# Optimization experiments

Measured on AMD Instinct MI355X. Metric: run time of the kernel, lower is better.

The kernel has to match this reference:

```python
import jax, jax.numpy as jnp
import numpy as np


def setup_inputs() -> dict:
    key = jax.random.key(0)
    ks = jax.random.split(key, 10)
    B, S, H = 8192, 8, 256
    SD, PD, AD = 9, 2, 7

    def lin(k, fan_in, shape):
        bound = 1.0 / np.sqrt(fan_in)
        return jax.random.uniform(k, shape, jnp.float32, -bound, bound)

    return {
        "state": jax.random.normal(ks[0], (B, SD), jnp.float32),
        "proprio": jax.random.normal(ks[1], (B, PD), jnp.float32),
        "target_pos": jax.random.normal(ks[2], (B, 3), jnp.float32),
        "noise": jax.random.normal(ks[3], (S, B, AD), jnp.float32),
        # action_proposal: Linear(11,H) -> ReLU -> Linear(H,7) -> Tanh
        "pw1": lin(ks[4], SD + PD, (SD + PD, H)),
        "pb1": jnp.zeros((H,), jnp.float32),
        "pw2": lin(ks[5], H, (H, AD)),
        "pb2": jnp.zeros((AD,), jnp.float32),
        # forward_model: Linear(16,H) -> ReLU -> Linear(H,H) -> ReLU -> Linear(H,9)
        "w1": lin(ks[6], SD + AD, (SD + AD, H)),
        "b1": jnp.zeros((H,), jnp.float32),
        "w2": lin(ks[7], H, (H, H)),
        "b2": jnp.zeros((H,), jnp.float32),
        "w3": lin(ks[8], H, (H, SD)),
        "b3": jnp.zeros((SD,), jnp.float32),
        "horizon": 4,
    }


def reference(state, proprio, target_pos, noise, pw1, pb1, pw2, pb2,
              w1, b1, w2, b2, w3, b3, horizon):
    # action proposal
    x = jnp.concatenate([state, proprio], axis=-1)          # (B, 11)
    base_action = jnp.tanh(jax.nn.relu(x @ pw1 + pb1) @ pw2 + pb2)  # (B, 7)

    # candidates for all samples at once (vectorizes the num_samples loop)
    cand = jnp.clip(base_action[None] + 0.2 * noise, -1.0, 1.0)      # (S, B, 7)

    S = cand.shape[0]
    sim0 = jnp.broadcast_to(state[None], (S,) + state.shape)         # (S, B, 9)

    def step(carry, _):
        sim, total = carry
        inp = jnp.concatenate([sim, cand], axis=-1)                  # (S, B, 16)
        h = jax.nn.relu(inp @ w1 + b1)
        h = jax.nn.relu(h @ w2 + b2)
        sim = h @ w3 + b3                                            # (S, B, 9)
        cost = jnp.sum((sim[..., :3] - target_pos[None]) ** 2, axis=-1)  # (S, B)
        return (sim, total + cost), None

    total0 = jnp.zeros(cand.shape[:2], jnp.float32)
    (_, total_cost), _ = jax.lax.scan(step, (sim0, total0), None, length=horizon)

    # masked best-cost update with strict '<' against +inf == first-argmin over samples
    best = jnp.argmin(total_cost, axis=0)                            # (B,)
    best_actions = jnp.take_along_axis(cand, best[None, :, None], axis=0)[0]  # (B, 7)
    return best_actions
```

## Files before the change

### kernel.cpp

```cpp
#include <hip/hip_runtime.h>
#include <math.h>

#define NSD 9
#define NPD 2
#define NAD 7
#define NH  256
#define NIN 16
#define LOSCALE 2048.0f
#define LOINV   (1.0f / 2048.0f)

typedef _Float16 half8 __attribute__((ext_vector_type(8)));
typedef float    floatx4 __attribute__((ext_vector_type(4)));


__device__ __forceinline__ void stage16(const _Float16* g, _Float16* l)
{
    __builtin_amdgcn_global_load_lds(
        (const __attribute__((address_space(1))) void*)g,
        (__attribute__((address_space(3))) void*)l, 16, 0, 0);
}

__global__ __launch_bounds__(64) void k_packW(
    const float* __restrict__ w1, const float* __restrict__ b1,
    const float* __restrict__ w2, const float* __restrict__ w3,
    _Float16* __restrict__ pc, _Float16* __restrict__ p3)
{
    const int bid  = blockIdx.x;
    const int lane = threadIdx.x;
    const int q = lane >> 4, ln = lane & 15;
    half8 hv, lv;
    _Float16* dst;
    if (bid < 16) {
        const int t = bid;
        const int c = 32*(t>>1) + 8*(ln>>2) + 4*(t&1) + (ln&3);
#pragma unroll
        for (int j = 0; j < 8; ++j) {
            const int k = 8*q + j;
            const float x = (k < NIN) ? w1[k*NH + c]
                                      : (k == NIN ? b1[c] : 0.0f);
            const _Float16 h = (_Float16)x;
            hv[j] = h; lv[j] = (_Float16)((x - (float)h) * LOSCALE);
        }
        dst = pc + (size_t)(t >> 1) * 18432 + 16384 + (size_t)(t & 1) * 1024;
    } else if (bid < 144) {
        const int idx = bid - 16, t = idx >> 3, kc = idx & 7;
        const int c = 32*(t>>1) + 8*(ln>>2) + 4*(t&1) + (ln&3);
#pragma unroll
        for (int j = 0; j < 8; ++j) {
            const int k = kc*32 + 8*q + j;
            const float x = w2[k*NH + c];
            const _Float16 h = (_Float16)x;
            hv[j] = h; lv[j] = (_Float16)((x - (float)h) * LOSCALE);
        }
        dst = pc + (size_t)kc * 18432 + (size_t)t * 1024;
    } else {
        const int kc = bid - 144;
#pragma unroll
        for (int j = 0; j < 8; ++j) {
            const int k = kc*32 + 8*q + j;
            const float x = (ln < NSD) ? w3[k*NSD + ln] : 0.0f;
            const _Float16 h = (_Float16)x;
            hv[j] = h; lv[j] = (_Float16)((x - (float)h) * LOSCALE);
        }
        dst = p3 + (size_t)kc * 1024;
    }
    *(half8*)&dst[lane*8]       = hv;
    *(half8*)&dst[512 + lane*8] = lv;
}

__global__ __launch_bounds__(256) void k_proposal(
    const float* __restrict__ state, const float* __restrict__ proprio,
    const float* __restrict__ noise, const float* __restrict__ pw1,
    const float* __restrict__ pb1, const float* __restrict__ pw2,
    const float* __restrict__ pb2, float* __restrict__ cand, int B)
{
    const int wave = threadIdx.x >> 6;
    const int lane = threadIdx.x & 63;
    const int b = blockIdx.x * 4 + wave;
    if (b >= B) return;

    float x[11];
#pragma unroll
    for (int k = 0; k < 9; ++k) x[k] = state[b * NSD + k];
    x[9]  = proprio[b * NPD + 0];
    x[10] = proprio[b * NPD + 1];

    float hc[4];
#pragma unroll
    for (int i = 0; i < 4; ++i) {
        const int c = lane + 64 * i;
        float acc = pb1[c];
#pragma unroll
        for (int k = 0; k < 11; ++k) acc = fmaf(x[k], pw1[k * NH + c], acc);
        hc[i] = fmaxf(acc, 0.0f);
    }

    float base[7];
#pragma unroll
    for (int j = 0; j < 7; ++j) {
        float p = 0.0f;
#pragma unroll
        for (int i = 0; i < 4; ++i)
            p = fmaf(hc[i], pw2[(lane + 64 * i) * NAD + j], p);
#pragma unroll
        for (int off = 32; off >= 1; off >>= 1) p += __shfl_xor(p, off, 64);
        base[j] = tanhf(p + pb2[j]);
    }

    if (lane < 8 * NAD) {
        const int s = lane / NAD, j = lane % NAD;
        float bj = base[0];
#pragma unroll
        for (int jj = 1; jj < 7; ++jj) if (j == jj) bj = base[jj];
        float v = bj + 0.2f * noise[((size_t)s * B + b) * NAD + j];
        v = fminf(fmaxf(v, -1.0f), 1.0f);
        cand[((size_t)s * B + b) * NAD + j] = v;
    }
}

__global__ __launch_bounds__(256, 2) void k_rollout(
    const float* __restrict__ state, const float* __restrict__ target,
    const float* __restrict__ cand,
    const _Float16* __restrict__ pc, const _Float16* __restrict__ p3,
    const float* __restrict__ b2, const float* __restrict__ b3,
    const int* __restrict__ hor_ptr, float* __restrict__ cost, int B)
{
    __shared__ _Float16 sb[2][18432];
    __shared__ float inpL[4][16][20];
    __shared__ float b2L[NH];

    const int tid  = threadIdx.x;
    const int wv   = tid >> 6;
    const int lane = tid & 63;
    const int q = lane >> 4, ln = lane & 15;
    const int chunk = blockIdx.x * 4 + wv;
    const int p0 = chunk * 16;
    const int s  = p0 / B;
    const int b0 = p0 % B;
    const int horizon = *hor_ptr;

    auto STAGE = [&](int buf, int kc) {
        const _Float16* gbase = pc + (size_t)kc * 18432 + tid * 8;
        _Float16* lbase = &sb[buf][wv * 512];
#pragma unroll
        for (int i = 0; i < 9; ++i)
            stage16(gbase + i * 2048, lbase + i * 2048);
    };

    b2L[tid] = b2[tid];
    if (q == 0) {
        float* row = &inpL[wv][ln][0];
        const int b = b0 + ln;
#pragma unroll
        for (int k = 0; k < NSD; ++k) row[k] = state[b * NSD + k];
#pragma unroll
        for (int j = 0; j < NAD; ++j)
            row[NSD + j] = cand[((size_t)s * B + b) * NAD + j];
        row[16] = 1.0f; row[17] = 0.0f; row[18] = 0.0f; row[19] = 0.0f;
    }
    float tg[3] = {0.0f, 0.0f, 0.0f};
    if (q == 0) {
#pragma unroll
        for (int r = 0; r < 3; ++r) tg[r] = target[(b0 + ln) * 3 + r];
    }
    float b3v[4];
#pragma unroll
    for (int r = 0; r < 4; ++r) {
        const int f = q * 4 + r;
        b3v[r] = (f < NSD) ? b3[f] : 0.0f;
    }
    float costAcc = 0.0f;

    STAGE(0, 0);
    asm volatile("s_waitcnt vmcnt(0)" ::: "memory");
    __syncthreads();
    int cur = 0;

    const floatx4 z4 = {0.0f, 0.0f, 0.0f, 0.0f};

    for (int h = 0; h < horizon; ++h) {
        const float* row = &inpL[wv][ln][0];
        float4 fa = {0, 0, 0, 0}, fb = {0, 0, 0, 0};
        if (q < 3) fa = *(const float4*)&row[8 * q];
        if (q < 2) fb = *(const float4*)&row[8 * q + 4];
        half8 bh, bl;
        {
            const float vv[8] = {fa.x, fa.y, fa.z, fa.w, fb.x, fb.y, fb.z, fb.w};
#pragma unroll
            for (int j = 0; j < 8; ++j) {
                const _Float16 hh = (_Float16)vv[j];
                bh[j] = hh;
                bl[j] = (_Float16)((vv[j] - (float)hh) * LOSCALE);
            }
        }

        floatx4 C1[16], C2[16];
#pragma unroll
        for (int t = 0; t < 16; ++t) { C1[t] = z4; C2[t] = z4; }

        for (int kc = 0; kc < 8; ++kc) {
            const int nkc = (kc < 7) ? kc + 1 : 0;
            STAGE(cur ^ 1, nkc);

            half8 h1h, h1l;
            {
                const half8 a1h0 = *(const half8*)&sb[cur][16384 + lane*8];
                const half8 a1l0 = *(const half8*)&sb[cur][16384 + 512 + lane*8];
                const half8 a1h1 = *(const half8*)&sb[cur][16384 + 1024 + lane*8];
                const half8 a1l1 = *(const half8*)&sb[cur][16384 + 1536 + lane*8];
                floatx4 c1t = __builtin_amdgcn_mfma_f32_16x16x32_f16(a1h0, bh, z4, 0, 0, 0);
                floatx4 c2t = __builtin_amdgcn_mfma_f32_16x16x32_f16(a1h0, bl, z4, 0, 0, 0);
                c2t = __builtin_amdgcn_mfma_f32_16x16x32_f16(a1l0, bh, c2t, 0, 0, 0);
#pragma unroll
                for (int r = 0; r < 4; ++r) {
                    const float v = fmaxf(fmaf(c2t[r], LOINV, c1t[r]), 0.0f);
                    const _Float16 hh = (_Float16)v;
                    h1h[r] = hh;
                    h1l[r] = (_Float16)((v - (float)hh) * LOSCALE);
                }
                c1t = __builtin_amdgcn_mfma_f32_16x16x32_f16(a1h1, bh, z4, 0, 0, 0);
                c2t = __builtin_amdgcn_mfma_f32_16x16x32_f16(a1h1, bl, z4, 0, 0, 0);
                c2t = __builtin_amdgcn_mfma_f32_16x16x32_f16(a1l1, bh, c2t, 0, 0, 0);
#pragma unroll
                for (int r = 0; r < 4; ++r) {
                    const float v = fmaxf(fmaf(c2t[r], LOINV, c1t[r]), 0.0f);
                    const _Float16 hh = (_Float16)v;
                    h1h[4 + r] = hh;
                    h1l[4 + r] = (_Float16)((v - (float)hh) * LOSCALE);
                }
            }

#pragma unroll
            for (int t = 0; t < 16; ++t) {
                const half8 a2h = *(const half8*)&sb[cur][t * 1024 + lane * 8];
                const half8 a2l = *(const half8*)&sb[cur][t * 1024 + 512 + lane * 8];
                C1[t] = __builtin_amdgcn_mfma_f32_16x16x32_f16(a2h, h1h, C1[t], 0, 0, 0);
                C2[t] = __builtin_amdgcn_mfma_f32_16x16x32_f16(a2h, h1l, C2[t], 0, 0, 0);
                C2[t] = __builtin_amdgcn_mfma_f32_16x16x32_f16(a2l, h1h, C2[t], 0, 0, 0);
            }

            __syncthreads();
            cur ^= 1;
        }

        floatx4 D1 = z4, D2 = z4;
        half8 h2h, h2l;
#pragma unroll
        for (int t = 0; t < 16; ++t) {
            const float4 bb = *(const float4*)&b2L[32*(t>>1) + 8*q + 4*(t&1)];
            const float bbv[4] = {bb.x, bb.y, bb.z, bb.w};
#pragma unroll
            for (int r = 0; r < 4; ++r) {
                const float v = fmaxf(C1[t][r] + LOINV * C2[t][r] + bbv[r], 0.0f);
                const _Float16 hh = (_Float16)v;
                h2h[(t & 1) * 4 + r] = hh;
                h2l[(t & 1) * 4 + r] = (_Float16)((v - (float)hh) * LOSCALE);
            }
            if (t & 1) {
                const int kc2 = t >> 1;
                const half8 a3h = *(const half8*)&p3[(size_t)kc2 * 1024 + lane*8];
                const half8 a3l = *(const half8*)&p3[(size_t)kc2 * 1024 + 512 + lane*8];
                D1 = __builtin_amdgcn_mfma_f32_16x16x32_f16(a3h, h2h, D1, 0, 0, 0);
                D2 = __builtin_amdgcn_mfma_f32_16x16x32_f16(a3h, h2l, D2, 0, 0, 0);
                D2 = __builtin_amdgcn_mfma_f32_16x16x32_f16(a3l, h2h, D2, 0, 0, 0);
            }
        }
        float v[4];
#pragma unroll
        for (int r = 0; r < 4; ++r)
            v[r] = D1[r] + LOINV * D2[r] + b3v[r];

        if (q == 0) {
            const float d0 = v[0] - tg[0], d1 = v[1] - tg[1], d2 = v[2] - tg[2];
            costAcc += d0 * d0 + d1 * d1 + d2 * d2;
        }
        if (q < 2) {
            const float4 w4 = {v[0], v[1], v[2], v[3]};
            *(float4*)&inpL[wv][ln][4 * q] = w4;
        } else if (q == 2) {
            inpL[wv][ln][8] = v[0];
        }
        asm volatile("s_waitcnt lgkmcnt(0)" ::: "memory");
    }

    if (q == 0) cost[(size_t)s * B + b0 + ln] = costAcc;
}

__global__ __launch_bounds__(256) void k_select(
    const float* __restrict__ cost, const float* __restrict__ cand,
    float* __restrict__ out, int B, int S)
{
    const int b = blockIdx.x * 256 + threadIdx.x;
    if (b >= B) return;
    float best = cost[b];
    int bs = 0;
    for (int s = 1; s < S; ++s) {
        const float c = cost[(size_t)s * B + b];
        if (c < best) { best = c; bs = s; }
    }
#pragma unroll
    for (int j = 0; j < NAD; ++j)
        out[b * NAD + j] = cand[((size_t)bs * B + b) * NAD + j];
}

extern "C" void kernel_launch(void* const* d_in, const int* in_sizes, int n_in,
                              void* d_out, int out_size, void* d_ws, size_t ws_size,
                              hipStream_t stream)
{
    const float* state   = (const float*)d_in[0];
    const float* proprio = (const float*)d_in[1];
    const float* target  = (const float*)d_in[2];
    const float* noise   = (const float*)d_in[3];
    const float* pw1     = (const float*)d_in[4];
    const float* pb1     = (const float*)d_in[5];
    const float* pw2     = (const float*)d_in[6];
    const float* pb2     = (const float*)d_in[7];
    const float* w1      = (const float*)d_in[8];
    const float* b1      = (const float*)d_in[9];
    const float* w2      = (const float*)d_in[10];
    const float* b2      = (const float*)d_in[11];
    const float* w3      = (const float*)d_in[12];
    const float* b3      = (const float*)d_in[13];
    const int*   horizon = (const int*)d_in[14];

    const int B = in_sizes[0] / NSD;
    const int S = in_sizes[3] / (B * NAD);

    float* cand = (float*)d_ws;
    float* cost = cand + (size_t)S * B * NAD;
    _Float16* pc = (_Float16*)(cost + (size_t)S * B);
    _Float16* p3 = pc + 8 * 18432;
    float* out  = (float*)d_out;

    k_packW<<<dim3(152), dim3(64), 0, stream>>>(w1, b1, w2, w3, pc, p3);
    k_proposal<<<dim3((B + 3) / 4), dim3(256), 0, stream>>>(
        state, proprio, noise, pw1, pb1, pw2, pb2, cand, B);
    k_rollout<<<dim3((S * B) / 64), dim3(256), 0, stream>>>(
        state, target, cand, pc, p3, b2, b3, horizon, cost, B);
    k_select<<<dim3((B + 255) / 256), dim3(256), 0, stream>>>(
        cost, cand, out, B, S);
}
```

Measured before the change: 221.7 us.

## Split layer-2 columns across wave pairs and merge weight-pack with proposal kernel

Each pair of waves now works on both waves' 16-sample chunks but only half of the 16 output tiles of the 256x256 layer. Each A-fragment loaded from LDS is therefore reused for two B operands, which halves LDS weight reads per MFMA. The partial layer-3 outputs are exchanged through shared memory with extra barriers each horizon step. Separately, the weight-packing and action-proposal kernels are fused into one launch to save a kernel launch.

```diff
diff --git a/kernel.cpp b/kernel.cpp
--- a/kernel.cpp
+++ b/kernel.cpp
@@ -8,6 +8,7 @@
 #define NIN 16
 #define LOSCALE 2048.0f
 #define LOINV   (1.0f / 2048.0f)
+#define NPACKB 152
 
 typedef _Float16 half8 __attribute__((ext_vector_type(8)));
 typedef float    floatx4 __attribute__((ext_vector_type(4)));
@@ -20,63 +21,65 @@
         (__attribute__((address_space(3))) void*)l, 16, 0, 0);
 }
 
-__global__ __launch_bounds__(64) void k_packW(
+__global__ __launch_bounds__(256) void k_prep(
     const float* __restrict__ w1, const float* __restrict__ b1,
     const float* __restrict__ w2, const float* __restrict__ w3,
-    _Float16* __restrict__ pc, _Float16* __restrict__ p3)
-{
-    const int bid  = blockIdx.x;
-    const int lane = threadIdx.x;
-    const int q = lane >> 4, ln = lane & 15;
-    half8 hv, lv;
-    _Float16* dst;
-    if (bid < 16) {
-        const int t = bid;
-        const int c = 32*(t>>1) + 8*(ln>>2) + 4*(t&1) + (ln&3);
-#pragma unroll
-        for (int j = 0; j < 8; ++j) {
-            const int k = 8*q + j;
-            const float x = (k < NIN) ? w1[k*NH + c]
-                                      : (k == NIN ? b1[c] : 0.0f);
-            const _Float16 h = (_Float16)x;
-            hv[j] = h; lv[j] = (_Float16)((x - (float)h) * LOSCALE);
-        }
-        dst = pc + (size_t)(t >> 1) * 18432 + 16384 + (size_t)(t & 1) * 1024;
-    } else if (bid < 144) {
-        const int idx = bid - 16, t = idx >> 3, kc = idx & 7;
-        const int c = 32*(t>>1) + 8*(ln>>2) + 4*(t&1) + (ln&3);
-#pragma unroll
-        for (int j = 0; j < 8; ++j) {
-            const int k = kc*32 + 8*q + j;
-            const float x = w2[k*NH + c];
-            const _Float16 h = (_Float16)x;
-            hv[j] = h; lv[j] = (_Float16)((x - (float)h) * LOSCALE);
-        }
-        dst = pc + (size_t)kc * 18432 + (size_t)t * 1024;
-    } else {
-        const int kc = bid - 144;
-#pragma unroll
-        for (int j = 0; j < 8; ++j) {
-            const int k = kc*32 + 8*q + j;
-            const float x = (ln < NSD) ? w3[k*NSD + ln] : 0.0f;
-            const _Float16 h = (_Float16)x;
-            hv[j] = h; lv[j] = (_Float16)((x - (float)h) * LOSCALE);
-        }
-        dst = p3 + (size_t)kc * 1024;
-    }
-    *(half8*)&dst[lane*8]       = hv;
-    *(half8*)&dst[512 + lane*8] = lv;
-}
-
-__global__ __launch_bounds__(256) void k_proposal(
+    _Float16* __restrict__ pc, _Float16* __restrict__ p3,
     const float* __restrict__ state, const float* __restrict__ proprio,
     const float* __restrict__ noise, const float* __restrict__ pw1,
     const float* __restrict__ pb1, const float* __restrict__ pw2,
     const float* __restrict__ pb2, float* __restrict__ cand, int B)
 {
+    const int bid = blockIdx.x;
+    if (bid < NPACKB) {
+        if (threadIdx.x >= 64) return;
+        const int lane = threadIdx.x;
+        const int q = lane >> 4, ln = lane & 15;
+        half8 hv, lv;
+        _Float16* dst;
+        if (bid < 16) {
+            const int t = bid;
+            const int c = 32*(t>>1) + 8*(ln>>2) + 4*(t&1) + (ln&3);
+#pragma unroll
+            for (int j = 0; j < 8; ++j) {
+                const int k = 8*q + j;
+                const float x = (k < NIN) ? w1[k*NH + c]
+                                          : (k == NIN ? b1[c] : 0.0f);
+                const _Float16 h = (_Float16)x;
+                hv[j] = h; lv[j] = (_Float16)((x - (float)h) * LOSCALE);
+            }
+            dst = pc + (size_t)(t >> 1) * 18432 + 16384 + (size_t)(t & 1) * 1024;
+        } else if (bid < 144) {
+            const int idx = bid - 16, t = idx >> 3, kc = idx & 7;
+            const int c = 32*(t>>1) + 8*(ln>>2) + 4*(t&1) + (ln&3);
+#pragma unroll
+            for (int j = 0; j < 8; ++j) {
+                const int k = kc*32 + 8*q + j;
+                const float x = w2[k*NH + c];
+                const _Float16 h = (_Float16)x;
+                hv[j] = h; lv[j] = (_Float16)((x - (float)h) * LOSCALE);
+            }
+            dst = pc + (size_t)kc * 18432 + (size_t)t * 1024;
+        } else {
+            const int kc = bid - 144;
+#pragma unroll
+            for (int j = 0; j < 8; ++j) {
+                const int k = kc*32 + 8*q + j;
+                const float x = (ln < NSD) ? w3[k*NSD + ln] : 0.0f;
+                const _Float16 h = (_Float16)x;
+                hv[j] = h; lv[j] = (_Float16)((x - (float)h) * LOSCALE);
+            }
+            dst = p3 + (size_t)kc * 1024;
+        }
+        *(half8*)&dst[lane*8]       = hv;
+        *(half8*)&dst[512 + lane*8] = lv;
+        return;
+    }
+
+    const int pbid = bid - NPACKB;
     const int wave = threadIdx.x >> 6;
     const int lane = threadIdx.x & 63;
-    const int b = blockIdx.x * 4 + wave;
+    const int b = pbid * 4 + wave;
     if (b >= B) return;
 
     float x[11];
@@ -133,6 +136,9 @@
     const int wv   = tid >> 6;
     const int lane = tid & 63;
     const int q = lane >> 4, ln = lane & 15;
+    const int wpair = wv & 2;
+    const int gown  = wv & 1;
+    const int tbase = gown * 8;
     const int chunk = blockIdx.x * 4 + wv;
     const int p0 = chunk * 16;
     const int s  = p0 / B;
@@ -179,96 +185,132 @@
     const floatx4 z4 = {0.0f, 0.0f, 0.0f, 0.0f};
 
     for (int h = 0; h < horizon; ++h) {
-        const float* row = &inpL[wv][ln][0];
-        float4 fa = {0, 0, 0, 0}, fb = {0, 0, 0, 0};
-        if (q < 3) fa = *(const float4*)&row[8 * q];
-        if (q < 2) fb = *(const float4*)&row[8 * q + 4];
-        half8 bh, bl;
-        {
+        half8 bh[2], bl[2];
+#pragma unroll
+        for (int g = 0; g < 2; ++g) {
+            const float* row = &inpL[wpair + g][ln][0];
+            float4 fa = {0, 0, 0, 0}, fb = {0, 0, 0, 0};
+            if (q < 3) fa = *(const float4*)&row[8 * q];
+            if (q < 2) fb = *(const float4*)&row[8 * q + 4];
             const float vv[8] = {fa.x, fa.y, fa.z, fa.w, fb.x, fb.y, fb.z, fb.w};
 #pragma unroll
             for (int j = 0; j < 8; ++j) {
                 const _Float16 hh = (_Float16)vv[j];
-                bh[j] = hh;
-                bl[j] = (_Float16)((vv[j] - (float)hh) * LOSCALE);
-            }
-        }
-
-        floatx4 C1[16], C2[16];
-#pragma unroll
-        for (int t = 0; t < 16; ++t) { C1[t] = z4; C2[t] = z4; }
+                bh[g][j] = hh;
+                bl[g][j] = (_Float16)((vv[j] - (float)hh) * LOSCALE);
+            }
+        }
+
+        floatx4 C1[8][2], C2[8][2];
+#pragma unroll
+        for (int tt = 0; tt < 8; ++tt)
+#pragma unroll
+            for (int g = 0; g < 2; ++g) { C1[tt][g] = z4; C2[tt][g] = z4; }
 
         for (int kc = 0; kc < 8; ++kc) {
             const int nkc = (kc < 7) ? kc + 1 : 0;
             STAGE(cur ^ 1, nkc);
 
-            half8 h1h, h1l;
-            {
-                const half8 a1h0 = *(const half8*)&sb[cur][16384 + lane*8];
-                const half8 a1l0 = *(const half8*)&sb[cur][16384 + 512 + lane*8];
-                const half8 a1h1 = *(const half8*)&sb[cur][16384 + 1024 + lane*8];
-                const half8 a1l1 = *(const half8*)&sb[cur][16384 + 1536 + lane*8];
-                floatx4 c1t = __builtin_amdgcn_mfma_f32_16x16x32_f16(a1h0, bh, z4, 0, 0, 0);
-                floatx4 c2t = __builtin_amdgcn_mfma_f32_16x16x32_f16(a1h0, bl, z4, 0, 0, 0);
-                c2t = __builtin_amdgcn_mfma_f32_16x16x32_f16(a1l0, bh, c2t, 0, 0, 0);
+            const half8 a1h0 = *(const half8*)&sb[cur][16384 + lane*8];
+            const half8 a1l0 = *(const half8*)&sb[cur][16384 + 512 + lane*8];
+            const half8 a1h1 = *(const half8*)&sb[cur][16384 + 1024 + lane*8];
+            const half8 a1l1 = *(const half8*)&sb[cur][16384 + 1536 + lane*8];
+            half8 h1h[2], h1l[2];
+#pragma unroll
+            for (int g = 0; g < 2; ++g) {
+                floatx4 c1t = __builtin_amdgcn_mfma_f32_16x16x32_f16(a1h0, bh[g], z4, 0, 0, 0);
+                floatx4 c2t = __builtin_amdgcn_mfma_f32_16x16x32_f16(a1h0, bl[g], z4, 0, 0, 0);
+                c2t = __builtin_amdgcn_mfma_f32_16x16x32_f16(a1l0, bh[g], c2t, 0, 0, 0);
 #pragma unroll
                 for (int r = 0; r < 4; ++r) {
                     const float v = fmaxf(fmaf(c2t[r], LOINV, c1t[r]), 0.0f);
                     const _Float16 hh = (_Float16)v;
-                    h1h[r] = hh;
-                    h1l[r] = (_Float16)((v - (float)hh) * LOSCALE);
-                }
-                c1t = __builtin_amdgcn_mfma_f32_16x16x32_f16(a1h1, bh, z4, 0, 0, 0);
-                c2t = __builtin_amdgcn_mfma_f32_16x16x32_f16(a1h1, bl, z4, 0, 0, 0);
-                c2t = __builtin_amdgcn_mfma_f32_16x16x32_f16(a1l1, bh, c2t, 0, 0, 0);
+                    h1h[g][r] = hh;
+                    h1l[g][r] = (_Float16)((v - (float)hh) * LOSCALE);
+                }
+                c1t = __builtin_amdgcn_mfma_f32_16x16x32_f16(a1h1, bh[g], z4, 0, 0, 0);
+                c2t = __builtin_amdgcn_mfma_f32_16x16x32_f16(a1h1, bl[g], z4, 0, 0, 0);
+                c2t = __builtin_amdgcn_mfma_f32_16x16x32_f16(a1l1, bh[g], c2t, 0, 0, 0);
 #pragma unroll
                 for (int r = 0; r < 4; ++r) {
                     const float v = fmaxf(fmaf(c2t[r], LOINV, c1t[r]), 0.0f);
                     const _Float16 hh = (_Float16)v;
-                    h1h[4 + r] = hh;
-                    h1l[4 + r] = (_Float16)((v - (float)hh) * LOSCALE);
-                }
-            }
-
-#pragma unroll
-            for (int t = 0; t < 16; ++t) {
+                    h1h[g][4 + r] = hh;
+                    h1l[g][4 + r] = (_Float16)((v - (float)hh) * LOSCALE);
+                }
+            }
+
+#pragma unroll
+            for (int tt = 0; tt < 8; ++tt) {
+                const int t = tbase + tt;
                 const half8 a2h = *(const half8*)&sb[cur][t * 1024 + lane * 8];
                 const half8 a2l = *(const half8*)&sb[cur][t * 1024 + 512 + lane * 8];
-                C1[t] = __builtin_amdgcn_mfma_f32_16x16x32_f16(a2h, h1h, C1[t], 0, 0, 0);
-                C2[t] = __builtin_amdgcn_mfma_f32_16x16x32_f16(a2h, h1l, C2[t], 0, 0, 0);
-                C2[t] = __builtin_amdgcn_mfma_f32_16x16x32_f16(a2l, h1h, C2[t], 0, 0, 0);
+#pragma unroll
+                for (int g = 0; g < 2; ++g) {
+                    C1[tt][g] = __builtin_amdgcn_mfma_f32_16x16x32_f16(a2h, h1h[g], C1[tt][g], 0, 0, 0);
+                    C2[tt][g] = __builtin_amdgcn_mfma_f32_16x16x32_f16(a2h, h1l[g], C2[tt][g], 0, 0, 0);
+                    C2[tt][g] = __builtin_amdgcn_mfma_f32_16x16x32_f16(a2l, h1h[g], C2[tt][g], 0, 0, 0);
+                }
             }
 
             __syncthreads();
             cur ^= 1;
         }
 
-        floatx4 D1 = z4, D2 = z4;
-        half8 h2h, h2l;
-#pragma unroll
-        for (int t = 0; t < 16; ++t) {
+        floatx4 D1[2] = {z4, z4}, D2[2] = {z4, z4};
+        half8 h2h[2], h2l[2];
+#pragma unroll
+        for (int tt = 0; tt < 8; ++tt) {
+            const int t = tbase + tt;
             const float4 bb = *(const float4*)&b2L[32*(t>>1) + 8*q + 4*(t&1)];
             const float bbv[4] = {bb.x, bb.y, bb.z, bb.w};
 #pragma unroll
-            for (int r = 0; r < 4; ++r) {
-                const float v = fmaxf(C1[t][r] + LOINV * C2[t][r] + bbv[r], 0.0f);
-                const _Float16 hh = (_Float16)v;
-                h2h[(t & 1) * 4 + r] = hh;
-                h2l[(t & 1) * 4 + r] = (_Float16)((v - (float)hh) * LOSCALE);
-            }
-            if (t & 1) {
+            for (int g = 0; g < 2; ++g)
+#pragma unroll
+                for (int r = 0; r < 4; ++r) {
+                    const float v = fmaxf(C1[tt][g][r] + LOINV * C2[tt][g][r] + bbv[r], 0.0f);
+                    const _Float16 hh = (_Float16)v;
+                    h2h[g][(tt & 1) * 4 + r] = hh;
+                    h2l[g][(tt & 1) * 4 + r] = (_Float16)((v - (float)hh) * LOSCALE);
+                }
+            if (tt & 1) {
                 const int kc2 = t >> 1;
                 const half8 a3h = *(const half8*)&p3[(size_t)kc2 * 1024 + lane*8];
                 const half8 a3l = *(const half8*)&p3[(size_t)kc2 * 1024 + 512 + lane*8];
-                D1 = __builtin_amdgcn_mfma_f32_16x16x32_f16(a3h, h2h, D1, 0, 0, 0);
-                D2 = __builtin_amdgcn_mfma_f32_16x16x32_f16(a3h, h2l, D2, 0, 0, 0);
-                D2 = __builtin_amdgcn_mfma_f32_16x16x32_f16(a3l, h2h, D2, 0, 0, 0);
-            }
-        }
+#pragma unroll
+                for (int g = 0; g < 2; ++g) {
+                    D1[g] = __builtin_amdgcn_mfma_f32_16x16x32_f16(a3h, h2h[g], D1[g], 0, 0, 0);
+                    D2[g] = __builtin_amdgcn_mfma_f32_16x16x32_f16(a3h, h2l[g], D2[g], 0, 0, 0);
+                    D2[g] = __builtin_amdgcn_mfma_f32_16x16x32_f16(a3l, h2h[g], D2[g], 0, 0, 0);
+                }
+            }
+        }
+
+        {
+            float* my = (float*)&sb[1][0] + wv * 512 + lane * 8;
+            float4 w1v, w2v;
+#pragma unroll
+            for (int r = 0; r < 4; ++r) {
+                w1v[r] = gown ? D1[0][r] : D1[1][r];
+                w2v[r] = gown ? D2[0][r] : D2[1][r];
+            }
+            *(float4*)&my[0] = w1v;
+            *(float4*)&my[4] = w2v;
+        }
+        __syncthreads();
+
         float v[4];
-#pragma unroll
-        for (int r = 0; r < 4; ++r)
-            v[r] = D1[r] + LOINV * D2[r] + b3v[r];
+        {
+            const float* pr = (const float*)&sb[1][0] + (wv ^ 1) * 512 + lane * 8;
+            const float4 p1v = *(const float4*)&pr[0];
+            const float4 p2v = *(const float4*)&pr[4];
+#pragma unroll
+            for (int r = 0; r < 4; ++r) {
+                const float o1 = gown ? D1[1][r] : D1[0][r];
+                const float o2 = gown ? D2[1][r] : D2[0][r];
+                v[r] = (o1 + p1v[r]) + LOINV * (o2 + p2v[r]) + b3v[r];
+            }
+        }
 
         if (q == 0) {
             const float d0 = v[0] - tg[0], d1 = v[1] - tg[1], d2 = v[2] - tg[2];
@@ -280,7 +322,7 @@
         } else if (q == 2) {
             inpL[wv][ln][8] = v[0];
         }
-        asm volatile("s_waitcnt lgkmcnt(0)" ::: "memory");
+        __syncthreads();
     }
 
     if (q == 0) cost[(size_t)s * B + b0 + ln] = costAcc;
@@ -332,8 +374,8 @@
     _Float16* p3 = pc + 8 * 18432;
     float* out  = (float*)d_out;
 
-    k_packW<<<dim3(152), dim3(64), 0, stream>>>(w1, b1, w2, w3, pc, p3);
-    k_proposal<<<dim3((B + 3) / 4), dim3(256), 0, stream>>>(
+    k_prep<<<dim3(NPACKB + (B + 3) / 4), dim3(256), 0, stream>>>(
+        w1, b1, w2, w3, pc, p3,
         state, proprio, noise, pw1, pb1, pw2, pb2, cand, B);
     k_rollout<<<dim3((S * B) / 64), dim3(256), 0, stream>>>(
         state, target, cand, pc, p3, b2, b3, horizon, cost, B);
```

Result: slower. 228.1 us (+2.9%).

## Split layer-2 output into two passes to halve LDS and accumulators; merge prep kernels

Applied to the files above, without the earlier changes.

The rollout kernel now computes the 256-wide second hidden layer in two 128-column passes. Each pass streams 8 smaller weight slices, so the double-buffered LDS footprint drops from about 72KB to 40KB and each wave holds 16 live accumulator tiles instead of 32, which lets launch bounds rise from 2 to 3 blocks per CU. The price is that layer-1 activations are recomputed in each pass, the w1 block is duplicated in the packed layout, and there are twice as many sync steps per horizon step. Separately, the weight-packing and proposal kernels are merged into one launch to save a kernel launch.

```diff
diff --git a/kernel.cpp b/kernel.cpp
--- a/kernel.cpp
+++ b/kernel.cpp
@@ -8,6 +8,8 @@
 #define NIN 16
 #define LOSCALE 2048.0f
 #define LOINV   (1.0f / 2048.0f)
+#define NPACKB 152
+#define SLICE 10240
 
 typedef _Float16 half8 __attribute__((ext_vector_type(8)));
 typedef float    floatx4 __attribute__((ext_vector_type(4)));
@@ -20,63 +22,73 @@
         (__attribute__((address_space(3))) void*)l, 16, 0, 0);
 }
 
-__global__ __launch_bounds__(64) void k_packW(
+__global__ __launch_bounds__(256) void k_prep(
     const float* __restrict__ w1, const float* __restrict__ b1,
     const float* __restrict__ w2, const float* __restrict__ w3,
-    _Float16* __restrict__ pc, _Float16* __restrict__ p3)
-{
-    const int bid  = blockIdx.x;
-    const int lane = threadIdx.x;
-    const int q = lane >> 4, ln = lane & 15;
-    half8 hv, lv;
-    _Float16* dst;
-    if (bid < 16) {
-        const int t = bid;
-        const int c = 32*(t>>1) + 8*(ln>>2) + 4*(t&1) + (ln&3);
-#pragma unroll
-        for (int j = 0; j < 8; ++j) {
-            const int k = 8*q + j;
-            const float x = (k < NIN) ? w1[k*NH + c]
-                                      : (k == NIN ? b1[c] : 0.0f);
-            const _Float16 h = (_Float16)x;
-            hv[j] = h; lv[j] = (_Float16)((x - (float)h) * LOSCALE);
-        }
-        dst = pc + (size_t)(t >> 1) * 18432 + 16384 + (size_t)(t & 1) * 1024;
-    } else if (bid < 144) {
-        const int idx = bid - 16, t = idx >> 3, kc = idx & 7;
-        const int c = 32*(t>>1) + 8*(ln>>2) + 4*(t&1) + (ln&3);
-#pragma unroll
-        for (int j = 0; j < 8; ++j) {
-            const int k = kc*32 + 8*q + j;
-            const float x = w2[k*NH + c];
-            const _Float16 h = (_Float16)x;
-            hv[j] = h; lv[j] = (_Float16)((x - (float)h) * LOSCALE);
-        }
-        dst = pc + (size_t)kc * 18432 + (size_t)t * 1024;
-    } else {
-        const int kc = bid - 144;
-#pragma unroll
-        for (int j = 0; j < 8; ++j) {
-            const int k = kc*32 + 8*q + j;
-            const float x = (ln < NSD) ? w3[k*NSD + ln] : 0.0f;
-            const _Float16 h = (_Float16)x;
-            hv[j] = h; lv[j] = (_Float16)((x - (float)h) * LOSCALE);
-        }
-        dst = p3 + (size_t)kc * 1024;
-    }
-    *(half8*)&dst[lane*8]       = hv;
-    *(half8*)&dst[512 + lane*8] = lv;
-}
-
-__global__ __launch_bounds__(256) void k_proposal(
+    _Float16* __restrict__ pc, _Float16* __restrict__ p3,
     const float* __restrict__ state, const float* __restrict__ proprio,
     const float* __restrict__ noise, const float* __restrict__ pw1,
     const float* __restrict__ pb1, const float* __restrict__ pw2,
     const float* __restrict__ pb2, float* __restrict__ cand, int B)
 {
+    const int bid = blockIdx.x;
+    if (bid < NPACKB) {
+        if (threadIdx.x >= 64) return;
+        const int lane = threadIdx.x;
+        const int q = lane >> 4, ln = lane & 15;
+        half8 hv, lv;
+        if (bid < 16) {
+            const int t = bid;
+            const int c = 32*(t>>1) + 8*(ln>>2) + 4*(t&1) + (ln&3);
+#pragma unroll
+            for (int j = 0; j < 8; ++j) {
+                const int k = 8*q + j;
+                const float x = (k < NIN) ? w1[k*NH + c]
+                                          : (k == NIN ? b1[c] : 0.0f);
+                const _Float16 h = (_Float16)x;
+                hv[j] = h; lv[j] = (_Float16)((x - (float)h) * LOSCALE);
+            }
+            const size_t off = 8192 + (size_t)(t & 1) * 1024;
+            _Float16* d0 = pc + (size_t)(t >> 1) * SLICE + off;
+            _Float16* d1 = pc + (size_t)(8 + (t >> 1)) * SLICE + off;
+            *(half8*)&d0[lane*8]       = hv;
+            *(half8*)&d0[512 + lane*8] = lv;
+            *(half8*)&d1[lane*8]       = hv;
+            *(half8*)&d1[512 + lane*8] = lv;
+            return;
+        }
+        _Float16* dst;
+        if (bid < 144) {
+            const int idx = bid - 16, t = idx >> 3, kc = idx & 7;
+            const int c = 32*(t>>1) + 8*(ln>>2) + 4*(t&1) + (ln&3);
+#pragma unroll
+            for (int j = 0; j < 8; ++j) {
+                const int k = kc*32 + 8*q + j;
+                const float x = w2[k*NH + c];
+                const _Float16 h = (_Float16)x;
+                hv[j] = h; lv[j] = (_Float16)((x - (float)h) * LOSCALE);
+            }
+            dst = pc + (size_t)((t >> 3) * 8 + kc) * SLICE + (size_t)(t & 7) * 1024;
+        } else {
+            const int kc = bid - 144;
+#pragma unroll
+            for (int j = 0; j < 8; ++j) {
+                const int k = kc*32 + 8*q + j;
+                const float x = (ln < NSD) ? w3[k*NSD + ln] : 0.0f;
+                const _Float16 h = (_Float16)x;
+                hv[j] = h; lv[j] = (_Float16)((x - (float)h) * LOSCALE);
+            }
+            dst = p3 + (size_t)kc * 1024;
+        }
+        *(half8*)&dst[lane*8]       = hv;
+        *(half8*)&dst[512 + lane*8] = lv;
+        return;
+    }
+
+    const int pbid = bid - NPACKB;
     const int wave = threadIdx.x >> 6;
     const int lane = threadIdx.x & 63;
-    const int b = blockIdx.x * 4 + wave;
+    const int b = pbid * 4 + wave;
     if (b >= B) return;
 
     float x[11];
@@ -118,14 +130,14 @@
     }
 }
 
-__global__ __launch_bounds__(256, 2) void k_rollout(
+__global__ __launch_bounds__(256, 3) void k_rollout(
     const float* __restrict__ state, const float* __restrict__ target,
     const float* __restrict__ cand,
     const _Float16* __restrict__ pc, const _Float16* __restrict__ p3,
     const float* __restrict__ b2, const float* __restrict__ b3,
     const int* __restrict__ hor_ptr, float* __restrict__ cost, int B)
 {
-    __shared__ _Float16 sb[2][18432];
+    __shared__ _Float16 sb[2][SLICE];
     __shared__ float inpL[4][16][20];
     __shared__ float b2L[NH];
 
@@ -139,11 +151,11 @@
     const int b0 = p0 % B;
     const int horizon = *hor_ptr;
 
-    auto STAGE = [&](int buf, int kc) {
-        const _Float16* gbase = pc + (size_t)kc * 18432 + tid * 8;
+    auto STAGE = [&](int buf, int sidx) {
+        const _Float16* gbase = pc + (size_t)sidx * SLICE + tid * 8;
         _Float16* lbase = &sb[buf][wv * 512];
 #pragma unroll
-        for (int i = 0; i < 9; ++i)
+        for (int i = 0; i < 5; ++i)
             stage16(gbase + i * 2048, lbase + i * 2048);
     };
 
@@ -174,7 +186,7 @@
     STAGE(0, 0);
     asm volatile("s_waitcnt vmcnt(0)" ::: "memory");
     __syncthreads();
-    int cur = 0;
+    int cur = 0, sidx = 0;
 
     const floatx4 z4 = {0.0f, 0.0f, 0.0f, 0.0f};
 
@@ -194,77 +206,84 @@
             }
         }
 
-        floatx4 C1[16], C2[16];
-#pragma unroll
-        for (int t = 0; t < 16; ++t) { C1[t] = z4; C2[t] = z4; }
-
-        for (int kc = 0; kc < 8; ++kc) {
-            const int nkc = (kc < 7) ? kc + 1 : 0;
-            STAGE(cur ^ 1, nkc);
-
-            half8 h1h, h1l;
-            {
-                const half8 a1h0 = *(const half8*)&sb[cur][16384 + lane*8];
-                const half8 a1l0 = *(const half8*)&sb[cur][16384 + 512 + lane*8];
-                const half8 a1h1 = *(const half8*)&sb[cur][16384 + 1024 + lane*8];
-                const half8 a1l1 = *(const half8*)&sb[cur][16384 + 1536 + lane*8];
-                floatx4 c1t = __builtin_amdgcn_mfma_f32_16x16x32_f16(a1h0, bh, z4, 0, 0, 0);
-                floatx4 c2t = __builtin_amdgcn_mfma_f32_16x16x32_f16(a1h0, bl, z4, 0, 0, 0);
-                c2t = __builtin_amdgcn_mfma_f32_16x16x32_f16(a1l0, bh, c2t, 0, 0, 0);
+        floatx4 D1 = z4, D2 = z4;
+
+#pragma unroll
+        for (int pass = 0; pass < 2; ++pass) {
+            floatx4 C1[8], C2[8];
+#pragma unroll
+            for (int tt = 0; tt < 8; ++tt) { C1[tt] = z4; C2[tt] = z4; }
+
+            for (int kc = 0; kc < 8; ++kc) {
+                const int nsidx = (sidx + 1) & 15;
+                STAGE(cur ^ 1, nsidx);
+
+                half8 h1h, h1l;
+                {
+                    const half8 a1h0 = *(const half8*)&sb[cur][8192 + lane*8];
+                    const half8 a1l0 = *(const half8*)&sb[cur][8192 + 512 + lane*8];
+                    const half8 a1h1 = *(const half8*)&sb[cur][8192 + 1024 + lane*8];
+                    const half8 a1l1 = *(const half8*)&sb[cur][8192 + 1536 + lane*8];
+                    floatx4 c1t = __builtin_amdgcn_mfma_f32_16x16x32_f16(a1h0, bh, z4, 0, 0, 0);
+                    floatx4 c2t = __builtin_amdgcn_mfma_f32_16x16x32_f16(a1h0, bl, z4, 0, 0, 0);
+                    c2t = __builtin_amdgcn_mfma_f32_16x16x32_f16(a1l0, bh, c2t, 0, 0, 0);
+#pragma unroll
+                    for (int r = 0; r < 4; ++r) {
+                        const float v = fmaxf(fmaf(c2t[r], LOINV, c1t[r]), 0.0f);
+                        const _Float16 hh = (_Float16)v;
+                        h1h[r] = hh;
+                        h1l[r] = (_Float16)((v - (float)hh) * LOSCALE);
+                    }
+                    c1t = __builtin_amdgcn_mfma_f32_16x16x32_f16(a1h1, bh, z4, 0, 0, 0);
+                    c2t = __builtin_amdgcn_mfma_f32_16x16x32_f16(a1h1, bl, z4, 0, 0, 0);
+                    c2t = __builtin_amdgcn_mfma_f32_16x16x32_f16(a1l1, bh, c2t, 0, 0, 0);
+#pragma unroll
+                    for (int r = 0; r < 4; ++r) {
+                        const float v = fmaxf(fmaf(c2t[r], LOINV, c1t[r]), 0.0f);
+                        const _Float16 hh = (_Float16)v;
+                        h1h[4 + r] = hh;
+                        h1l[4 + r] = (_Float16)((v - (float)hh) * LOSCALE);
+                    }
+                }
+
+#pragma unroll
+                for (int tt = 0; tt < 8; ++tt) {
+                    const half8 a2h = *(const half8*)&sb[cur][tt * 1024 + lane * 8];
+                    const half8 a2l = *(const half8*)&sb[cur][tt * 1024 + 512 + lane * 8];
+                    C1[tt] = __builtin_amdgcn_mfma_f32_16x16x32_f16(a2h, h1h, C1[tt], 0, 0, 0);
+                    C2[tt] = __builtin_amdgcn_mfma_f32_16x16x32_f16(a2h, h1l, C2[tt], 0, 0, 0);
+                    C2[tt] = __builtin_amdgcn_mfma_f32_16x16x32_f16(a2l, h1h, C2[tt], 0, 0, 0);
+                }
+
+                __syncthreads();
+                cur ^= 1;
+                sidx = nsidx;
+            }
+
+            half8 h2h, h2l;
+#pragma unroll
+            for (int tt = 0; tt < 8; ++tt) {
+                const int t = pass * 8 + tt;
+                const float4 bb = *(const float4*)&b2L[32*(t>>1) + 8*q + 4*(t&1)];
+                const float bbv[4] = {bb.x, bb.y, bb.z, bb.w};
 #pragma unroll
                 for (int r = 0; r < 4; ++r) {
-                    const float v = fmaxf(fmaf(c2t[r], LOINV, c1t[r]), 0.0f);
+                    const float v = fmaxf(C1[tt][r] + LOINV * C2[tt][r] + bbv[r], 0.0f);
                     const _Float16 hh = (_Float16)v;
-                    h1h[r] = hh;
-                    h1l[r] = (_Float16)((v - (float)hh) * LOSCALE);
+                    h2h[(tt & 1) * 4 + r] = hh;
+                    h2l[(tt & 1) * 4 + r] = (_Float16)((v - (float)hh) * LOSCALE);
                 }
-                c1t = __builtin_amdgcn_mfma_f32_16x16x32_f16(a1h1, bh, z4, 0, 0, 0);
-                c2t = __builtin_amdgcn_mfma_f32_16x16x32_f16(a1h1, bl, z4, 0, 0, 0);
-                c2t = __builtin_amdgcn_mfma_f32_16x16x32_f16(a1l1, bh, c2t, 0, 0, 0);
-#pragma unroll
-                for (int r = 0; r < 4; ++r) {
-                    const float v = fmaxf(fmaf(c2t[r], LOINV, c1t[r]), 0.0f);
-                    const _Float16 hh = (_Float16)v;
-                    h1h[4 + r] = hh;
-                    h1l[4 + r] = (_Float16)((v - (float)hh) * LOSCALE);
+                if (tt & 1) {
+                    const int kc2 = t >> 1;
+                    const half8 a3h = *(const half8*)&p3[(size_t)kc2 * 1024 + lane*8];
+                    const half8 a3l = *(const half8*)&p3[(size_t)kc2 * 1024 + 512 + lane*8];
+                    D1 = __builtin_amdgcn_mfma_f32_16x16x32_f16(a3h, h2h, D1, 0, 0, 0);
+                    D2 = __builtin_amdgcn_mfma_f32_16x16x32_f16(a3h, h2l, D2, 0, 0, 0);
+                    D2 = __builtin_amdgcn_mfma_f32_16x16x32_f16(a3l, h2h, D2, 0, 0, 0);
                 }
             }
-
-#pragma unroll
-            for (int t = 0; t < 16; ++t) {
-                const half8 a2h = *(const half8*)&sb[cur][t * 1024 + lane * 8];
-                const half8 a2l = *(const half8*)&sb[cur][t * 1024 + 512 + lane * 8];
-                C1[t] = __builtin_amdgcn_mfma_f32_16x16x32_f16(a2h, h1h, C1[t], 0, 0, 0);
-                C2[t] = __builtin_amdgcn_mfma_f32_16x16x32_f16(a2h, h1l, C2[t], 0, 0, 0);
-                C2[t] = __builtin_amdgcn_mfma_f32_16x16x32_f16(a2l, h1h, C2[t], 0, 0, 0);
-            }
-
-            __syncthreads();
-            cur ^= 1;
-        }
-
-        floatx4 D1 = z4, D2 = z4;
-        half8 h2h, h2l;
-#pragma unroll
-        for (int t = 0; t < 16; ++t) {
-            const float4 bb = *(const float4*)&b2L[32*(t>>1) + 8*q + 4*(t&1)];
-            const float bbv[4] = {bb.x, bb.y, bb.z, bb.w};
-#pragma unroll
-            for (int r = 0; r < 4; ++r) {
-                const float v = fmaxf(C1[t][r] + LOINV * C2[t][r] + bbv[r], 0.0f);
-                const _Float16 hh = (_Float16)v;
-                h2h[(t & 1) * 4 + r] = hh;
-                h2l[(t & 1) * 4 + r] = (_Float16)((v - (float)hh) * LOSCALE);
-            }
-            if (t & 1) {
-                const int kc2 = t >> 1;
-                const half8 a3h = *(const half8*)&p3[(size_t)kc2 * 1024 + lane*8];
-                const half8 a3l = *(const half8*)&p3[(size_t)kc2 * 1024 + 512 + lane*8];
-                D1 = __builtin_amdgcn_mfma_f32_16x16x32_f16(a3h, h2h, D1, 0, 0, 0);
-                D2 = __builtin_amdgcn_mfma_f32_16x16x32_f16(a3h, h2l, D2, 0, 0, 0);
-                D2 = __builtin_amdgcn_mfma_f32_16x16x32_f16(a3l, h2h, D2, 0, 0, 0);
-            }
-        }
+        }
+
         float v[4];
 #pragma unroll
         for (int r = 0; r < 4; ++r)
@@ -329,11 +348,11 @@
     float* cand = (float*)d_ws;
     float* cost = cand + (size_t)S * B * NAD;
     _Float16* pc = (_Float16*)(cost + (size_t)S * B);
-    _Float16* p3 = pc + 8 * 18432;
+    _Float16* p3 = pc + 16 * SLICE;
     float* out  = (float*)d_out;
 
-    k_packW<<<dim3(152), dim3(64), 0, stream>>>(w1, b1, w2, w3, pc, p3);
-    k_proposal<<<dim3((B + 3) / 4), dim3(256), 0, stream>>>(
+    k_prep<<<dim3(NPACKB + (B + 3) / 4), dim3(256), 0, stream>>>(
+        w1, b1, w2, w3, pc, p3,
         state, proprio, noise, pw1, pb1, pw2, pb2, cand, B);
     k_rollout<<<dim3((S * B) / 64), dim3(256), 0, stream>>>(
         state, target, cand, pc, p3, b2, b3, horizon, cost, B);
```

New measurement: 255.4 us. 15.2% more time.
